# Optimization experiments

Measured on AMD Instinct MI355X. Metric: run time of the kernel, lower is better.

## Reference

```python
import jax, jax.numpy as jnp
import numpy as np

N = 50000        # nodes
E = 400000       # edges
SC = 64          # scalar (l=0) channels
VC = 32          # vector (l=1) channels
DIM = SC + 3 * VC  # 160
NB = 64          # radial basis functions
CUTOFF = 5.0
EPS = 1e-5


def _edge_rot_mat(edge_vec, edge_rand):
    # init_edge_rot_mat: build per-edge frame aligning edge dir with canonical axis
    dist = jnp.sqrt(jnp.sum(edge_vec ** 2, axis=1, keepdims=True))
    nx = edge_vec / dist
    ev2 = edge_rand - 0.5
    ev2 = ev2 / jnp.sqrt(jnp.sum(ev2 ** 2, axis=1, keepdims=True))
    ev2b = jnp.stack([-ev2[:, 1], ev2[:, 0], ev2[:, 2]], axis=1)
    ev2c = jnp.stack([ev2[:, 0], -ev2[:, 2], ev2[:, 1]], axis=1)
    dot = lambda a: jnp.abs(jnp.sum(a * nx, axis=1, keepdims=True))
    ev2 = jnp.where(dot(ev2) > dot(ev2b), ev2b, ev2)
    ev2 = jnp.where(dot(ev2) > dot(ev2c), ev2c, ev2)
    nz = jnp.cross(nx, ev2)
    nz = nz / jnp.sqrt(jnp.sum(nz ** 2, axis=1, keepdims=True))
    ny = jnp.cross(nx, nz)
    ny = ny / jnp.sqrt(jnp.sum(ny ** 2, axis=1, keepdims=True))
    # edge_rot_mat_inv columns = [nz, nx, -ny]; R = inv^T -> rows = [nz, nx, -ny]
    return jnp.stack([nz, nx, -ny], axis=1)  # [E,3,3]


def setup_inputs() -> dict:
    key = jax.random.key(0)
    ks = jax.random.split(key, 10)
    x = jax.random.normal(ks[0], (N, DIM), dtype=jnp.float32)
    pos = jax.random.normal(ks[1], (N, 3), dtype=jnp.float32)
    src = jax.random.randint(ks[2], (E,), 0, N)
    off = jax.random.randint(ks[3], (E,), 1, N)
    dst = (src + off) % N  # no self loops -> nonzero edge vectors
    edge_index = jnp.stack([src, dst], axis=0).astype(jnp.int64)
    edge_rand = jax.random.uniform(ks[4], (E, 3), dtype=jnp.float32)
    W0 = jax.random.normal(ks[5], (SC, SC), dtype=jnp.float32)
    W1 = jax.random.normal(ks[6], (VC, VC), dtype=jnp.float32)
    rbf_centers = jnp.linspace(0.0, CUTOFF, NB).astype(jnp.float32)
    rbf_widths = 0.5 * jnp.ones((NB,), dtype=jnp.float32)
    edge_proj_w = 0.1 * jax.random.normal(ks[7], (NB, 1), dtype=jnp.float32)
    edge_proj_b = jnp.zeros((1,), dtype=jnp.float32)
    ln_gamma = jnp.ones((SC,), dtype=jnp.float32) + 0.1 * jax.random.normal(ks[8], (SC,), dtype=jnp.float32)
    ln_beta = 0.1 * jax.random.normal(ks[9], (SC,), dtype=jnp.float32)
    return {"x": x, "pos": pos, "edge_index": edge_index, "edge_rand": edge_rand,
            "W0": W0, "W1": W1, "rbf_centers": rbf_centers, "rbf_widths": rbf_widths,
            "edge_proj_w": edge_proj_w, "edge_proj_b": edge_proj_b,
            "ln_gamma": ln_gamma, "ln_beta": ln_beta}


def reference(x, pos, edge_index, edge_rand, W0, W1, rbf_centers, rbf_widths,
              edge_proj_w, edge_proj_b, ln_gamma, ln_beta):
    src, dst = edge_index[0], edge_index[1]
    edge_vec = pos[src] - pos[dst]                       # [E,3]
    dist = jnp.sqrt(jnp.sum(edge_vec ** 2, axis=1))      # [E]
    # rotation matrices are detached in the original
    R = jax.lax.stop_gradient(_edge_rot_mat(edge_vec, edge_rand))  # [E,3,3]

    # radial basis (gaussian) with cosine cutoff envelope
    d = dist[:, None]                                    # [E,1]
    rbf = jnp.exp(-0.5 * ((d - rbf_centers) / rbf_widths) ** 2)  # [E,NB]
    cut = jnp.where(d <= CUTOFF, 0.5 * (jnp.cos(jnp.pi * d / CUTOFF) + 1.0), 0.0)
    rbf = rbf * cut                                      # [E,NB]

    # gather source features, split irreps 64x0e + 32x1e
    h = x[src]                                           # [E,DIM]
    h0 = h[:, :SC]                                       # [E,SC]
    h1 = h[:, SC:].reshape(-1, VC, 3)                    # [E,VC,3]

    # rotate l=1 block into the edge-aligned frame (Wigner-D for l=1 is R)
    h1r = jnp.einsum('eij,ecj->eci', R, h1)

    # SO2 convolution: per-l channel mixing (o3.Linear, 1/sqrt(fan_in) path norm)
    m0 = (h0 @ W0) / np.sqrt(SC)                         # [E,SC]
    m1 = jnp.einsum('ecj,cd->edj', h1r, W1) / np.sqrt(VC)  # [E,VC,3]

    # edge modulation: global mean of sigmoid(edge_proj(rbf)) (scalar, as in source)
    edge_w = jnp.mean(jax.nn.sigmoid(rbf @ edge_proj_w + edge_proj_b))
    m0 = m0 * edge_w
    m1 = m1 * edge_w

    # rotate l=1 back with R^T
    m1b = jnp.einsum('eji,ecj->eci', R, m1)
    msg = jnp.concatenate([m0, m1b.reshape(-1, 3 * VC)], axis=1)  # [E,DIM]

    # scatter-sum aggregation over destination nodes
    agg = jax.ops.segment_sum(msg, dst, num_segments=x.shape[0])  # [N,DIM]

    # EquivariantLayerNormV2: LayerNorm on l=0 slice only
    s = agg[:, :SC]
    mu = jnp.mean(s, axis=-1, keepdims=True)
    var = jnp.mean((s - mu) ** 2, axis=-1, keepdims=True)
    s_ln = (s - mu) / jnp.sqrt(var + EPS) * ln_gamma + ln_beta

    # S2Activation: SiLU on l=0 slice, identity on l=1
    s_act = jax.nn.silu(s_ln)
    return jnp.concatenate([s_act, agg[:, SC:]], axis=1)  # [N,DIM]
```

## Files before the change

### kernel.cpp

```cpp
#include <hip/hip_runtime.h>

#define N_NODES 50000
#define N_EDGES 400000
#define DIM 160
#define NB 64
#define CUTOFF 5.0f
#define LN_EPS 1e-5f
#define PI_F 3.14159265358979323846f

#define SLOT_STRIDE 64

#define DEG_STRIDE 4

#define WS_DEG   16
#define WS_PKT   (WS_DEG + N_NODES * DEG_STRIDE)
#define WS_POS4  (WS_PKT + 4 * NB)
#define WS_ESRC  (WS_POS4 + 4 * N_NODES)

__global__ __launch_bounds__(256) void prep(
    const float* __restrict__ pos, const float* __restrict__ centers,
    const float* __restrict__ widths, const float* __restrict__ proj_w,
    int* __restrict__ degp, float4* __restrict__ pkt,
    float4* __restrict__ pos4, float* __restrict__ ew_accum)
{
    const int i = blockIdx.x * blockDim.x + threadIdx.x;
    if (i < 16) ((int*)ew_accum)[i] = 0;
    if (i < NB)
        pkt[i] = make_float4(centers[i], 1.0f / widths[i], proj_w[i], 0.0f);
    if (i < N_NODES) {
        ((int4*)(degp))[i] = make_int4(0, 0, 0, 0);
        pos4[i] = make_float4(pos[3 * i], pos[3 * i + 1], pos[3 * i + 2], 0.0f);
    }
}

#define EPT 4

__global__ __launch_bounds__(256) void hist_ew_fill(
    const int* __restrict__ ei, const float4* __restrict__ pos4,
    const float4* __restrict__ pkt, const float* __restrict__ proj_b,
    int* __restrict__ degp, int* __restrict__ esrc, float* __restrict__ ew_accum)
{
    const float bias = proj_b[0];
    const int base = blockIdx.x * (256 * EPT) + threadIdx.x;

    int  s[EPT], d[EPT], slot[EPT];
    bool v[EPT];
    #pragma unroll
    for (int k = 0; k < EPT; ++k) {
        const int e = base + 256 * k;
        v[k] = (e < N_EDGES);
        s[k] = v[k] ? ei[e] : 0;
        d[k] = v[k] ? ei[N_EDGES + e] : 0;
    }

    #pragma unroll
    for (int k = 0; k < EPT; ++k)
        slot[k] = v[k] ? atomicAdd(&degp[(long)d[k] * DEG_STRIDE], 1) : 0;

    float4 ps[EPT], pd[EPT];
    #pragma unroll
    for (int k = 0; k < EPT; ++k) { ps[k] = pos4[s[k]]; pd[k] = pos4[d[k]]; }

    #pragma unroll
    for (int k = 0; k < EPT; ++k)
        if (v[k] && slot[k] < SLOT_STRIDE)
            esrc[((long)d[k] << 6) + slot[k]] = s[k];

    float dist[EPT];
    #pragma unroll
    for (int k = 0; k < EPT; ++k) {
        const float dx = ps[k].x - pd[k].x;
        const float dy = ps[k].y - pd[k].y;
        const float dz = ps[k].z - pd[k].z;
        dist[k] = sqrtf(dx * dx + dy * dy + dz * dz);
    }

    float z[EPT] = {0.f, 0.f, 0.f, 0.f};
    #pragma unroll 4
    for (int b = 0; b < NB; ++b) {
        const float4 t4 = pkt[b];
        #pragma unroll
        for (int k = 0; k < EPT; ++k) {
            const float t = (dist[k] - t4.x) * t4.y;
            z[k] = fmaf(__expf(-0.5f * t * t), t4.z, z[k]);
        }
    }

    float sig = 0.0f;
    #pragma unroll
    for (int k = 0; k < EPT; ++k) {
        if (v[k]) {
            const float cut = (dist[k] <= CUTOFF)
                            ? 0.5f * (__cosf(PI_F * dist[k] * (1.0f / CUTOFF)) + 1.0f)
                            : 0.0f;
            sig += 1.0f / (1.0f + __expf(-(z[k] * cut + bias)));
        }
    }

    #pragma unroll
    for (int off = 32; off > 0; off >>= 1) sig += __shfl_xor(sig, off);
    __shared__ float red[4];
    if ((threadIdx.x & 63) == 0) red[threadIdx.x >> 6] = sig;
    __syncthreads();
    if (threadIdx.x == 0)
        atomicAdd(ew_accum, red[0] + red[1] + red[2] + red[3]);
}

#define GNODES 32

__global__ __launch_bounds__(256) void gather_pass(
    const float* __restrict__ x, const int* __restrict__ degp,
    const int* __restrict__ esrc, float* __restrict__ agg)
{
    const int node0 = blockIdx.x * GNODES;
    #pragma unroll
    for (int it = 0; it < 5; ++it) {
        const int t2 = it * 256 + threadIdx.x;
        const int nl = t2 / 40;
        const int c  = t2 - nl * 40;
        const int n  = node0 + nl;
        if (n >= N_NODES) continue;

        const int cnt = min(degp[(long)n * DEG_STRIDE], SLOT_STRIDE);
        const int4* sl4 = (const int4*)(esrc + ((long)n << 6));
        const int4 sa = sl4[0];
        const int4 sb = sl4[1];
        const int4 sc = sl4[2];
        const int4 sd = sl4[3];
        const int sj[16] = { sa.x, sa.y, sa.z, sa.w,  sb.x, sb.y, sb.z, sb.w,
                             sc.x, sc.y, sc.z, sc.w,  sd.x, sd.y, sd.z, sd.w };

        float4 acc = make_float4(0.f, 0.f, 0.f, 0.f);
        #pragma unroll
        for (int j = 0; j < 16; ++j) {
            if (j < cnt) {
                const float4 v = *(const float4*)(x + (long)sj[j] * DIM + 4 * c);
                acc.x += v.x; acc.y += v.y; acc.z += v.z; acc.w += v.w;
            }
        }
        for (int j = 16; j < cnt; ++j) {
            const int s = esrc[((long)n << 6) + j];
            const float4 v = *(const float4*)(x + (long)s * DIM + 4 * c);
            acc.x += v.x; acc.y += v.y; acc.z += v.z; acc.w += v.w;
        }
        *(float4*)(agg + (long)n * DIM + 4 * c) = acc;
    }
}

#define ROWP 164
#define TNODES 64

__global__ __launch_bounds__(256) void node_tiled(
    float* __restrict__ agg,
    const float* __restrict__ W0, const float* __restrict__ W1,
    const float* __restrict__ ln_gamma, const float* __restrict__ ln_beta,
    const float* __restrict__ ew_accum)
{
    __shared__ float sA[TNODES * ROWP];
    __shared__ float sW0[64 * 64];
    __shared__ float sW1[32 * 32];

    const int t = threadIdx.x;
    const int node0 = blockIdx.x * TNODES;

    {
        const float4* w04 = (const float4*)W0;
        float4* s04 = (float4*)sW0;
        #pragma unroll
        for (int i = 0; i < 4; ++i) s04[t + 256 * i] = w04[t + 256 * i];
        ((float4*)sW1)[t] = ((const float4*)W1)[t];
    }
    {
        #pragma unroll
        for (int i = 0; i < 10; ++i) {
            const int idx = t + 256 * i;
            const int r   = idx / 40;
            const int c4  = idx - r * 40;
            const int n   = node0 + r;
            float4 v = make_float4(0.f, 0.f, 0.f, 0.f);
            if (n < N_NODES) v = ((const float4*)(agg + (long)n * DIM))[c4];
            *(float4*)(&sA[r * ROWP + 4 * c4]) = v;
        }
    }
    __syncthreads();

    const float ew   = ew_accum[0] * (1.0f / 400000.0f);
    const float s_m0 = ew * 0.125f;
    const float s_m1 = ew * 0.17677669529663687f;

    {
        const int q   = t >> 4;
        const int sub = t & 15;
        const float* r0 = sA + (4 * q + 0) * ROWP;
        const float* r1 = sA + (4 * q + 1) * ROWP;
        const float* r2 = sA + (4 * q + 2) * ROWP;
        const float* r3 = sA + (4 * q + 3) * ROWP;

        float acc[4][4];
        #pragma unroll
        for (int n = 0; n < 4; ++n)
            #pragma unroll
            for (int j = 0; j < 4; ++j) acc[n][j] = 0.0f;

        #pragma unroll 4
        for (int k0 = 0; k0 < 64; k0 += 4) {
            const float4 a0 = *(const float4*)(r0 + k0);
            const float4 a1 = *(const float4*)(r1 + k0);
            const float4 a2 = *(const float4*)(r2 + k0);
            const float4 a3 = *(const float4*)(r3 + k0);
            const float4 w0 = *(const float4*)(sW0 + (k0 + 0) * 64 + 4 * sub);
            const float4 w1 = *(const float4*)(sW0 + (k0 + 1) * 64 + 4 * sub);
            const float4 w2 = *(const float4*)(sW0 + (k0 + 2) * 64 + 4 * sub);
            const float4 w3 = *(const float4*)(sW0 + (k0 + 3) * 64 + 4 * sub);
            #define FMA4(A, av, wv) \
                A[0] = fmaf(av, wv.x, A[0]); A[1] = fmaf(av, wv.y, A[1]); \
                A[2] = fmaf(av, wv.z, A[2]); A[3] = fmaf(av, wv.w, A[3]);
            FMA4(acc[0], a0.x, w0) FMA4(acc[0], a0.y, w1) FMA4(acc[0], a0.z, w2) FMA4(acc[0], a0.w, w3)
            FMA4(acc[1], a1.x, w0) FMA4(acc[1], a1.y, w1) FMA4(acc[1], a1.z, w2) FMA4(acc[1], a1.w, w3)
            FMA4(acc[2], a2.x, w0) FMA4(acc[2], a2.y, w1) FMA4(acc[2], a2.z, w2) FMA4(acc[2], a2.w, w3)
            FMA4(acc[3], a3.x, w0) FMA4(acc[3], a3.y, w1) FMA4(acc[3], a3.z, w2) FMA4(acc[3], a3.w, w3)
            #undef FMA4
        }

        float sum[4], ssq[4];
        #pragma unroll
        for (int n = 0; n < 4; ++n) {
            sum[n] = 0.0f; ssq[n] = 0.0f;
            #pragma unroll
            for (int j = 0; j < 4; ++j) {
                acc[n][j] *= s_m0;
                sum[n] += acc[n][j];
                ssq[n] = fmaf(acc[n][j], acc[n][j], ssq[n]);
            }
        }
        #pragma unroll
        for (int m = 1; m <= 8; m <<= 1) {
            #pragma unroll
            for (int n = 0; n < 4; ++n) {
                sum[n] += __shfl_xor(sum[n], m);
                ssq[n] += __shfl_xor(ssq[n], m);
            }
        }

        const float4 g = *(const float4*)(ln_gamma + 4 * sub);
        const float4 b = *(const float4*)(ln_beta  + 4 * sub);
        #pragma unroll
        for (int n = 0; n < 4; ++n) {
            const int node = node0 + 4 * q + n;
            if (node < N_NODES) {
                const float mu   = sum[n] * (1.0f / 64.0f);
                const float var  = ssq[n] * (1.0f / 64.0f) - mu * mu;
                const float rstd = rsqrtf(var + LN_EPS);
                const float t0 = (acc[n][0] - mu) * rstd * g.x + b.x;
                const float t1 = (acc[n][1] - mu) * rstd * g.y + b.y;
                const float t2 = (acc[n][2] - mu) * rstd * g.z + b.z;
                const float t3 = (acc[n][3] - mu) * rstd * g.w + b.w;
                float4 o;
                o.x = t0 / (1.0f + __expf(-t0));
                o.y = t1 / (1.0f + __expf(-t1));
                o.z = t2 / (1.0f + __expf(-t2));
                o.w = t3 / (1.0f + __expf(-t3));
                *(float4*)(agg + (long)node * DIM + 4 * sub) = o;
            }
        }
    }

    {
        const int nl   = t >> 2;
        const int sub  = t & 3;
        const int node = node0 + nl;
        const bool valid = node < N_NODES;
        float* grow = agg + (long)(valid ? node : 0) * DIM;
        const float* aRow = sA + nl * ROWP;

        float o[24];
        #pragma unroll
        for (int m = 0; m < 24; ++m) o[m] = 0.0f;

        const float* bRow = aRow + 64;
        #pragma unroll 2
        for (int tt = 0; tt < 8; ++tt) {
            const float4 v0 = *(const float4*)(bRow + 12 * tt);
            const float4 v1 = *(const float4*)(bRow + 12 * tt + 4);
            const float4 v2 = *(const float4*)(bRow + 12 * tt + 8);
            const float a[12] = { v0.x, v0.y, v0.z, v0.w,
                                  v1.x, v1.y, v1.z, v1.w,
                                  v2.x, v2.y, v2.z, v2.w };
            #pragma unroll
            for (int r = 0; r < 4; ++r) {
                const int cp = 4 * tt + r;
                const float a0 = a[3 * r];
                const float a1 = a[3 * r + 1];
                const float a2 = a[3 * r + 2];
                const float4* w4 = (const float4*)(sW1 + cp * 32 + sub * 8);
                const float4 wA = w4[0];
                const float4 wB = w4[1];
                const float wc[8] = { wA.x, wA.y, wA.z, wA.w, wB.x, wB.y, wB.z, wB.w };
                #pragma unroll
                for (int cc = 0; cc < 8; ++cc) {
                    o[3 * cc]     = fmaf(wc[cc], a0, o[3 * cc]);
                    o[3 * cc + 1] = fmaf(wc[cc], a1, o[3 * cc + 1]);
                    o[3 * cc + 2] = fmaf(wc[cc], a2, o[3 * cc + 2]);
                }
            }
        }

        if (valid) {
            float4* ro4 = (float4*)(grow + 64 + 24 * sub);
            #pragma unroll
            for (int q2 = 0; q2 < 6; ++q2) {
                float4 ov;
                ov.x = o[4 * q2]     * s_m1;
                ov.y = o[4 * q2 + 1] * s_m1;
                ov.z = o[4 * q2 + 2] * s_m1;
                ov.w = o[4 * q2 + 3] * s_m1;
                ro4[q2] = ov;
            }
        }
    }
}

extern "C" void kernel_launch(void* const* d_in, const int* in_sizes, int n_in,
                              void* d_out, int out_size, void* d_ws, size_t ws_size,
                              hipStream_t stream) {
    const float* x       = (const float*)d_in[0];
    const float* pos     = (const float*)d_in[1];
    const int*   ei      = (const int*)d_in[2];
    const float* W0      = (const float*)d_in[4];
    const float* W1      = (const float*)d_in[5];
    const float* centers = (const float*)d_in[6];
    const float* widths  = (const float*)d_in[7];
    const float* proj_w  = (const float*)d_in[8];
    const float* proj_b  = (const float*)d_in[9];
    const float* gamma   = (const float*)d_in[10];
    const float* beta    = (const float*)d_in[11];

    float* out  = (float*)d_out;
    int*   wsi  = (int*)d_ws;
    float* ew   = (float*)d_ws;
    int*   degp = wsi + WS_DEG;
    float4* pkt  = (float4*)(wsi + WS_PKT);
    float4* pos4 = (float4*)(wsi + WS_POS4);
    int*   esrc = wsi + WS_ESRC;

    const int pb = (N_NODES + 255) / 256;
    prep<<<pb, 256, 0, stream>>>(pos, centers, widths, proj_w, degp, pkt, pos4, ew);

    const int eb = (N_EDGES + 256 * EPT - 1) / (256 * EPT);
    hist_ew_fill<<<eb, 256, 0, stream>>>(ei, pos4, pkt, proj_b, degp, esrc, ew);

    const int gb = (N_NODES + GNODES - 1) / GNODES;
    gather_pass<<<gb, 256, 0, stream>>>(x, degp, esrc, out);

    const int tiles = (N_NODES + TNODES - 1) / TNODES;
    node_tiled<<<tiles, 256, 0, stream>>>(out, W0, W1, gamma, beta, ew);
}
```

Before: 201.1 us.

## Fuse neighbor gather into node tile kernel, gathering directly into shared memory

Removes the separate gather_pass kernel. Each wavefront of the node kernel now gathers 16 nodes' neighbor sums straight into the shared tile, reading source indices once per lane and broadcasting them with shuffles. This saves the write and re-read of the intermediate aggregate array plus one launch, and unrolls the gather eight deep for memory-level parallelism. In exchange, only 40 of 64 lanes do useful loads, and the gather now runs under the node kernel's heavier LDS and register footprint, which may lower occupancy.

Result: no change. 200.9 us (-0.1%).

```diff
diff --git a/kernel.cpp b/kernel.cpp
--- a/kernel.cpp
+++ b/kernel.cpp
@@ -9,7 +9,6 @@
 #define PI_F 3.14159265358979323846f
 
 #define SLOT_STRIDE 64
-
 #define DEG_STRIDE 4
 
 #define WS_DEG   16
@@ -106,52 +105,12 @@
         atomicAdd(ew_accum, red[0] + red[1] + red[2] + red[3]);
 }
 
-#define GNODES 32
-
-__global__ __launch_bounds__(256) void gather_pass(
-    const float* __restrict__ x, const int* __restrict__ degp,
-    const int* __restrict__ esrc, float* __restrict__ agg)
-{
-    const int node0 = blockIdx.x * GNODES;
-    #pragma unroll
-    for (int it = 0; it < 5; ++it) {
-        const int t2 = it * 256 + threadIdx.x;
-        const int nl = t2 / 40;
-        const int c  = t2 - nl * 40;
-        const int n  = node0 + nl;
-        if (n >= N_NODES) continue;
-
-        const int cnt = min(degp[(long)n * DEG_STRIDE], SLOT_STRIDE);
-        const int4* sl4 = (const int4*)(esrc + ((long)n << 6));
-        const int4 sa = sl4[0];
-        const int4 sb = sl4[1];
-        const int4 sc = sl4[2];
-        const int4 sd = sl4[3];
-        const int sj[16] = { sa.x, sa.y, sa.z, sa.w,  sb.x, sb.y, sb.z, sb.w,
-                             sc.x, sc.y, sc.z, sc.w,  sd.x, sd.y, sd.z, sd.w };
-
-        float4 acc = make_float4(0.f, 0.f, 0.f, 0.f);
-        #pragma unroll
-        for (int j = 0; j < 16; ++j) {
-            if (j < cnt) {
-                const float4 v = *(const float4*)(x + (long)sj[j] * DIM + 4 * c);
-                acc.x += v.x; acc.y += v.y; acc.z += v.z; acc.w += v.w;
-            }
-        }
-        for (int j = 16; j < cnt; ++j) {
-            const int s = esrc[((long)n << 6) + j];
-            const float4 v = *(const float4*)(x + (long)s * DIM + 4 * c);
-            acc.x += v.x; acc.y += v.y; acc.z += v.z; acc.w += v.w;
-        }
-        *(float4*)(agg + (long)n * DIM + 4 * c) = acc;
-    }
-}
-
 #define ROWP 164
 #define TNODES 64
 
-__global__ __launch_bounds__(256) void node_tiled(
-    float* __restrict__ agg,
+__global__ __launch_bounds__(256) void gather_node_fused(
+    const float* __restrict__ x, const int* __restrict__ degp,
+    const int* __restrict__ esrc, float* __restrict__ out,
     const float* __restrict__ W0, const float* __restrict__ W1,
     const float* __restrict__ ln_gamma, const float* __restrict__ ln_beta,
     const float* __restrict__ ew_accum)
@@ -160,27 +119,99 @@
     __shared__ float sW0[64 * 64];
     __shared__ float sW1[32 * 32];
 
-    const int t = threadIdx.x;
+    const int t    = threadIdx.x;
+    const int lane = t & 63;
+    const int w    = t >> 6;
     const int node0 = blockIdx.x * TNODES;
 
+    float4 w0r[4];
+    #pragma unroll
+    for (int i = 0; i < 4; ++i) w0r[i] = ((const float4*)W0)[t + 256 * i];
+    const float4 w1r = ((const float4*)W1)[t];
+
+    #pragma unroll 1
+    for (int p = 0; p < 16; p += 2) {
+        const int nlA = w * 16 + p;
+        const int nlB = nlA + 1;
+        const int nA  = node0 + nlA;
+        const int nB  = node0 + nlB;
+        const long nAc = (nA < N_NODES) ? nA : 0;
+        const long nBc = (nB < N_NODES) ? nB : 0;
+
+        const int svA  = esrc[(nAc << 6) + lane];
+        const int svB  = esrc[(nBc << 6) + lane];
+        const int cntA = (nA < N_NODES) ? min(degp[nAc * DEG_STRIDE], SLOT_STRIDE) : 0;
+        const int cntB = (nB < N_NODES) ? min(degp[nBc * DEG_STRIDE], SLOT_STRIDE) : 0;
+
+        float4 aA = make_float4(0.f, 0.f, 0.f, 0.f);
+        float4 aB = make_float4(0.f, 0.f, 0.f, 0.f);
+
+        #define GBODY(sv, cnt, acc)                                            \
+        {                                                                      \
+            int j = 0;                                                         \
+            for (; j + 8 <= cnt; j += 8) {                                     \
+                const int s0 = __shfl(sv, j);                                  \
+                const int s1 = __shfl(sv, j + 1);                              \
+                const int s2 = __shfl(sv, j + 2);                              \
+                const int s3 = __shfl(sv, j + 3);                              \
+                const int s4 = __shfl(sv, j + 4);                              \
+                const int s5 = __shfl(sv, j + 5);                              \
+                const int s6 = __shfl(sv, j + 6);                              \
+                const int s7 = __shfl(sv, j + 7);                              \
+                if (lane < 40) {                                               \
+                    const float4 v0 = ((const float4*)(x + (long)s0 * DIM))[lane]; \
+                    const float4 v1 = ((const float4*)(x + (long)s1 * DIM))[lane]; \
+                    const float4 v2 = ((const float4*)(x + (long)s2 * DIM))[lane]; \
+                    const float4 v3 = ((const float4*)(x + (long)s3 * DIM))[lane]; \
+                    const float4 v4 = ((const float4*)(x + (long)s4 * DIM))[lane]; \
+                    const float4 v5 = ((const float4*)(x + (long)s5 * DIM))[lane]; \
+                    const float4 v6 = ((const float4*)(x + (long)s6 * DIM))[lane]; \
+                    const float4 v7 = ((const float4*)(x + (long)s7 * DIM))[lane]; \
+                    acc.x += ((v0.x + v1.x) + (v2.x + v3.x)) + ((v4.x + v5.x) + (v6.x + v7.x)); \
+                    acc.y += ((v0.y + v1.y) + (v2.y + v3.y)) + ((v4.y + v5.y) + (v6.y + v7.y)); \
+                    acc.z += ((v0.z + v1.z) + (v2.z + v3.z)) + ((v4.z + v5.z) + (v6.z + v7.z)); \
+                    acc.w += ((v0.w + v1.w) + (v2.w + v3.w)) + ((v4.w + v5.w) + (v6.w + v7.w)); \
+                }                                                              \
+            }                                                                  \
+            for (; j + 4 <= cnt; j += 4) {                                     \
+                const int s0 = __shfl(sv, j);                                  \
+                const int s1 = __shfl(sv, j + 1);                              \
+                const int s2 = __shfl(sv, j + 2);                              \
+                const int s3 = __shfl(sv, j + 3);                              \
+                if (lane < 40) {                                               \
+                    const float4 v0 = ((const float4*)(x + (long)s0 * DIM))[lane]; \
+                    const float4 v1 = ((const float4*)(x + (long)s1 * DIM))[lane]; \
+                    const float4 v2 = ((const float4*)(x + (long)s2 * DIM))[lane]; \
+                    const float4 v3 = ((const float4*)(x + (long)s3 * DIM))[lane]; \
+                    acc.x += (v0.x + v1.x) + (v2.x + v3.x);                    \
+                    acc.y += (v0.y + v1.y) + (v2.y + v3.y);                    \
+                    acc.z += (v0.z + v1.z) + (v2.z + v3.z);                    \
+                    acc.w += (v0.w + v1.w) + (v2.w + v3.w);                    \
+                }                                                              \
+            }                                                                  \
+            for (; j < cnt; ++j) {                                             \
+                const int s0 = __shfl(sv, j);                                  \
+                if (lane < 40) {                                               \
+                    const float4 v0 = ((const float4*)(x + (long)s0 * DIM))[lane]; \
+                    acc.x += v0.x; acc.y += v0.y; acc.z += v0.z; acc.w += v0.w; \
+                }                                                              \
+            }                                                                  \
+        }
+        GBODY(svA, cntA, aA)
+        GBODY(svB, cntB, aB)
+        #undef GBODY
+
+        if (lane < 40) {
+            *(float4*)(&sA[nlA * ROWP + 4 * lane]) = aA;
+            *(float4*)(&sA[nlB * ROWP + 4 * lane]) = aB;
+        }
+    }
+
     {
-        const float4* w04 = (const float4*)W0;
         float4* s04 = (float4*)sW0;
         #pragma unroll
-        for (int i = 0; i < 4; ++i) s04[t + 256 * i] = w04[t + 256 * i];
-        ((float4*)sW1)[t] = ((const float4*)W1)[t];
-    }
-    {
-        #pragma unroll
-        for (int i = 0; i < 10; ++i) {
-            const int idx = t + 256 * i;
-            const int r   = idx / 40;
-            const int c4  = idx - r * 40;
-            const int n   = node0 + r;
-            float4 v = make_float4(0.f, 0.f, 0.f, 0.f);
-            if (n < N_NODES) v = ((const float4*)(agg + (long)n * DIM))[c4];
-            *(float4*)(&sA[r * ROWP + 4 * c4]) = v;
-        }
+        for (int i = 0; i < 4; ++i) s04[t + 256 * i] = w0r[i];
+        ((float4*)sW1)[t] = w1r;
     }
     __syncthreads();
 
@@ -260,7 +291,7 @@
                 o.y = t1 / (1.0f + __expf(-t1));
                 o.z = t2 / (1.0f + __expf(-t2));
                 o.w = t3 / (1.0f + __expf(-t3));
-                *(float4*)(agg + (long)node * DIM + 4 * sub) = o;
+                *(float4*)(out + (long)node * DIM + 4 * sub) = o;
             }
         }
     }
@@ -270,7 +301,7 @@
         const int sub  = t & 3;
         const int node = node0 + nl;
         const bool valid = node < N_NODES;
-        float* grow = agg + (long)(valid ? node : 0) * DIM;
+        float* grow = out + (long)(valid ? node : 0) * DIM;
         const float* aRow = sA + nl * ROWP;
 
         float o[24];
@@ -349,9 +380,7 @@
     const int eb = (N_EDGES + 256 * EPT - 1) / (256 * EPT);
     hist_ew_fill<<<eb, 256, 0, stream>>>(ei, pos4, pkt, proj_b, degp, esrc, ew);
 
-    const int gb = (N_NODES + GNODES - 1) / GNODES;
-    gather_pass<<<gb, 256, 0, stream>>>(x, degp, esrc, out);
-
     const int tiles = (N_NODES + TNODES - 1) / TNODES;
-    node_tiled<<<tiles, 256, 0, stream>>>(out, W0, W1, gamma, beta, ew);
+    gather_node_fused<<<tiles, 256, 0, stream>>>(x, degp, esrc, out,
+                                                 W0, W1, gamma, beta, ew);
 }
```
